# Kernel tuning notes

Hardware: AMD Instinct MI355X
Metric: run time of the kernel (lower is better)

Reference implementation:

```python
import jax, jax.numpy as jnp
import numpy as np

DIM = 512
HEADS = 16
WIN = (8, 8)
N = WIN[0] * WIN[1]  # 64 tokens per window
BW = 1024            # batch * num_windows
TABLE = (2 * WIN[0] - 1) * (2 * WIN[1] - 1)  # 225


def _relative_position_index():
    ch, cw = np.arange(WIN[0]), np.arange(WIN[1])
    coords = np.stack(np.meshgrid(ch, cw, indexing='ij'))        # [2,Wh,Ww]
    flat = coords.reshape(2, -1)                                  # [2,N]
    rel = flat[:, :, None] - flat[:, None, :]                     # [2,N,N]
    rel = rel.transpose(1, 2, 0).astype(np.int64)                 # [N,N,2]
    rel[:, :, 0] += WIN[0] - 1
    rel[:, :, 1] += WIN[1] - 1
    rel[:, :, 0] *= 2 * WIN[1] - 1
    return jnp.asarray(rel.sum(-1), dtype=jnp.int32)              # [N,N]


def setup_inputs() -> dict:
    key = jax.random.key(0)
    ks = jax.random.split(key, 8)
    s = 0.02
    return {
        'q': jax.random.normal(ks[0], (BW, N, DIM), jnp.float32),
        'wq': jax.random.normal(ks[1], (DIM, DIM), jnp.float32) * s,
        'bq': jnp.zeros((DIM,), jnp.float32),
        'wkv': jax.random.normal(ks[2], (DIM, 2 * DIM), jnp.float32) * s,
        'bkv': jnp.zeros((2 * DIM,), jnp.float32),
        'wproj': jax.random.normal(ks[3], (DIM, DIM), jnp.float32) * s,
        'bproj': jnp.zeros((DIM,), jnp.float32),
        'bias_table': jax.random.normal(ks[4], (TABLE, HEADS), jnp.float32) * s,
        'rel_pos_index': _relative_position_index(),
    }


def reference(q, wq, bq, wkv, bkv, wproj, bproj, bias_table, rel_pos_index):
    B, n, C = q.shape
    hd = C // HEADS
    scale = hd ** -0.5
    # projections (torch Linear with pre-transposed weights)
    qh = (q @ wq + bq).reshape(B, n, HEADS, hd).transpose(0, 2, 1, 3) * scale  # [B,H,N,hd]
    kv = (q @ wkv + bkv).reshape(B, n, 2, HEADS, hd)
    k = kv[:, :, 0].transpose(0, 2, 1, 3)  # [B,H,N,hd]
    v = kv[:, :, 1].transpose(0, 2, 1, 3)
    attn = jnp.einsum('bhqd,bhkd->bhqk', qh, k)                   # [B,H,N,N]
    bias = bias_table[rel_pos_index].transpose(2, 0, 1)           # [H,N,N]
    attn = jax.nn.softmax(attn + bias[None], axis=-1)
    x = jnp.einsum('bhqk,bhkd->bqhd', attn, v).reshape(B, n, C)
    x = x @ wproj + bproj
    return x, attn
```

## Files before the change

### kernel.cpp

```cpp
#include <hip/hip_runtime.h>
#include <hip/hip_bf16.h>
#include <stdint.h>

typedef __attribute__((ext_vector_type(8))) __bf16 bf16x8;
typedef __attribute__((ext_vector_type(4))) float f32x4;

#define MFMA16(a, b, c) __builtin_amdgcn_mfma_f32_16x16x32_bf16(a, b, c, 0, 0, 0)

__device__ __forceinline__ void gload16(const void* g, void* l) {
  __builtin_amdgcn_global_load_lds((const __attribute__((address_space(1))) void*)g,
                                   (__attribute__((address_space(3))) void*)l, 16, 0, 0);
}

__global__ __launch_bounds__(256) void prep_kernel(
    const float* __restrict__ wq, const float* __restrict__ bq,
    const float* __restrict__ wkv, const float* __restrict__ bkv,
    const float* __restrict__ wproj, const float* __restrict__ btab,
    const int* __restrict__ relidx,
    __bf16* __restrict__ W1t, __bf16* __restrict__ WpT,
    float* __restrict__ bias1, float* __restrict__ bias_frag) {
  const float scale = 0.17677669529663687f;
  int t = blockIdx.x * 256 + threadIdx.x;
  if (t < 786432) {
    int j = t >> 9, kk = t & 511;
    float v = (j < 512) ? wq[kk * 512 + j] * scale : wkv[kk * 1024 + (j - 512)];
    W1t[t] = (__bf16)v;
  } else if (t < 1048576) {
    int u = t - 786432;
    int j = u >> 9, kk = u & 511;
    WpT[u] = (__bf16)wproj[kk * 512 + j];
  } else if (t < 1050112) {
    int j = t - 1048576;
    bias1[j] = (j < 512) ? bq[j] * scale : bkv[j - 512];
  } else if (t < 1115648) {
    int u = t - 1050112;
    int r = u & 3, l = (u >> 2) & 63, nj = (u >> 8) & 3, mi = (u >> 10) & 3, h = u >> 12;
    int qq = mi * 16 + (l >> 4) * 4 + r;
    int nn = nj * 16 + (l & 15);
    bias_frag[u] = btab[relidx[qq * 64 + nn] * 16 + h];
  }
}

__global__ __launch_bounds__(256) void cvt_kernel(const float* __restrict__ in,
                                                  __bf16* __restrict__ out) {
  int t = blockIdx.x * 256 + threadIdx.x;
  const float4* p = (const float4*)in + (size_t)t * 2;
  float4 a = p[0], b = p[1];
  bf16x8 v = {(__bf16)a.x, (__bf16)a.y, (__bf16)a.z, (__bf16)a.w,
              (__bf16)b.x, (__bf16)b.y, (__bf16)b.z, (__bf16)b.w};
  *((bf16x8*)out + t) = v;
}

__global__ __launch_bounds__(256) void gemm1_kernel(
    const __bf16* __restrict__ A, const __bf16* __restrict__ W1t,
    const float* __restrict__ bias1,
    __bf16* __restrict__ qh, __bf16* __restrict__ kb, __bf16* __restrict__ vT) {
  __shared__ __bf16 As[128 * 32];
  __shared__ __bf16 Bs[128 * 32];
  int tid = threadIdx.x;
  int w = tid >> 6, l = tid & 63, c = l & 15, g = l >> 4;
  int wm = w >> 1, wn = w & 1;
  int bx = blockIdx.x, by = blockIdx.y;
  int r0 = by * 128, n0 = bx * 128;

  f32x4 acc[4][4] = {};
  int e0 = w * 1024 + l * 8;
  int rn0 = e0 >> 5, rk0 = e0 & 31;
  int e1 = e0 + 512;
  int rn1 = e1 >> 5, rk1 = e1 & 31;

  for (int kt = 0; kt < 16; ++kt) {
    int k0 = kt * 32;
    __syncthreads();
    gload16(A + (size_t)(r0 + rn0) * 512 + k0 + rk0, (void*)(As + w * 1024));
    gload16(A + (size_t)(r0 + rn1) * 512 + k0 + rk1, (void*)(As + w * 1024 + 512));
    gload16(W1t + (size_t)(n0 + rn0) * 512 + k0 + rk0, (void*)(Bs + w * 1024));
    gload16(W1t + (size_t)(n0 + rn1) * 512 + k0 + rk1, (void*)(Bs + w * 1024 + 512));
    __syncthreads();
    bf16x8 af[4], bfr[4];
#pragma unroll
    for (int mi = 0; mi < 4; mi++) af[mi] = *(const bf16x8*)(As + (wm * 64 + mi * 16 + c) * 32 + g * 8);
#pragma unroll
    for (int nj = 0; nj < 4; nj++) bfr[nj] = *(const bf16x8*)(Bs + (wn * 64 + nj * 16 + c) * 32 + g * 8);
#pragma unroll
    for (int mi = 0; mi < 4; mi++)
#pragma unroll
      for (int nj = 0; nj < 4; nj++)
        acc[mi][nj] = MFMA16(af[mi], bfr[nj], acc[mi][nj]);
  }

  float bia[4];
#pragma unroll
  for (int nj = 0; nj < 4; nj++) bia[nj] = bias1[n0 + wn * 64 + nj * 16 + c];
  int rowbase = r0 + wm * 64 + g * 4;
  int colbase = n0 + wn * 64 + c;
#pragma unroll
  for (int mi = 0; mi < 4; mi++) {
#pragma unroll
    for (int nj = 0; nj < 4; nj++) {
      int col = colbase + nj * 16;
      int jj = col & 511;
      int h = jj >> 5, d = jj & 31;
#pragma unroll
      for (int r = 0; r < 4; r++) {
        int row = rowbase + mi * 16 + r;
        int b = row >> 6, tok = row & 63;
        float val = acc[mi][nj][r] + bia[nj];
        size_t base = (size_t)(b * 16 + h) * 2048;
        if (bx < 4)
          qh[base + tok * 32 + d] = (__bf16)val;
        else if (bx < 8)
          kb[base + tok * 32 + d] = (__bf16)val;
        else
          vT[base + d * 64 + tok] = (__bf16)val;
      }
    }
  }
}

__global__ __launch_bounds__(64) void attn_kernel(
    const __bf16* __restrict__ qh, const __bf16* __restrict__ kb,
    const __bf16* __restrict__ vT, const float* __restrict__ bias_frag,
    float* __restrict__ attn_out, __bf16* __restrict__ xpart) {
  __shared__ __bf16 P[64 * 72];
  int bh = blockIdx.x;
  int b = bh >> 4, h = bh & 15;
  int l = threadIdx.x, c = l & 15, g = l >> 4;
  const __bf16* qp = qh + (size_t)bh * 2048;
  const __bf16* kp = kb + (size_t)bh * 2048;
  const __bf16* vp = vT + (size_t)bh * 2048;

  bf16x8 af[4], bfr[4];
#pragma unroll
  for (int mi = 0; mi < 4; mi++) af[mi] = *(const bf16x8*)(qp + (mi * 16 + c) * 32 + g * 8);
#pragma unroll
  for (int nj = 0; nj < 4; nj++) bfr[nj] = *(const bf16x8*)(kp + (nj * 16 + c) * 32 + g * 8);

  f32x4 acc[4][4];
#pragma unroll
  for (int mi = 0; mi < 4; mi++)
#pragma unroll
    for (int nj = 0; nj < 4; nj++)
      acc[mi][nj] = *(const f32x4*)(bias_frag + ((size_t)((h * 4 + mi) * 4 + nj) * 64 + l) * 4);
#pragma unroll
  for (int mi = 0; mi < 4; mi++)
#pragma unroll
    for (int nj = 0; nj < 4; nj++)
      acc[mi][nj] = MFMA16(af[mi], bfr[nj], acc[mi][nj]);

  float* ao = attn_out + (size_t)bh * 4096;
#pragma unroll
  for (int mi = 0; mi < 4; mi++) {
#pragma unroll
    for (int r = 0; r < 4; r++) {
      float m = fmaxf(fmaxf(acc[mi][0][r], acc[mi][1][r]), fmaxf(acc[mi][2][r], acc[mi][3][r]));
      m = fmaxf(m, __shfl_xor(m, 1));
      m = fmaxf(m, __shfl_xor(m, 2));
      m = fmaxf(m, __shfl_xor(m, 4));
      m = fmaxf(m, __shfl_xor(m, 8));
      float p0 = __expf(acc[mi][0][r] - m);
      float p1 = __expf(acc[mi][1][r] - m);
      float p2 = __expf(acc[mi][2][r] - m);
      float p3 = __expf(acc[mi][3][r] - m);
      float s = p0 + p1 + p2 + p3;
      s += __shfl_xor(s, 1);
      s += __shfl_xor(s, 2);
      s += __shfl_xor(s, 4);
      s += __shfl_xor(s, 8);
      float rs = 1.0f / s;
      p0 *= rs; p1 *= rs; p2 *= rs; p3 *= rs;
      int row = mi * 16 + g * 4 + r;
      ao[row * 64 + c] = p0;
      ao[row * 64 + 16 + c] = p1;
      ao[row * 64 + 32 + c] = p2;
      ao[row * 64 + 48 + c] = p3;
      P[row * 72 + c] = (__bf16)p0;
      P[row * 72 + 16 + c] = (__bf16)p1;
      P[row * 72 + 32 + c] = (__bf16)p2;
      P[row * 72 + 48 + c] = (__bf16)p3;
    }
  }
  __syncthreads();

  bf16x8 pa[4][2];
#pragma unroll
  for (int mi = 0; mi < 4; mi++)
#pragma unroll
    for (int kk = 0; kk < 2; kk++)
      pa[mi][kk] = *(const bf16x8*)(P + (mi * 16 + c) * 72 + kk * 32 + g * 8);
  bf16x8 bv[2][2];
#pragma unroll
  for (int dj = 0; dj < 2; dj++)
#pragma unroll
    for (int kk = 0; kk < 2; kk++)
      bv[dj][kk] = *(const bf16x8*)(vp + (c + 16 * dj) * 64 + kk * 32 + g * 8);
  f32x4 xacc[4][2] = {};
#pragma unroll
  for (int mi = 0; mi < 4; mi++)
#pragma unroll
    for (int dj = 0; dj < 2; dj++)
#pragma unroll
      for (int kk = 0; kk < 2; kk++)
        xacc[mi][dj] = MFMA16(pa[mi][kk], bv[dj][kk], xacc[mi][dj]);

  __bf16* xp = xpart + (size_t)b * 64 * 512 + h * 32;
#pragma unroll
  for (int mi = 0; mi < 4; mi++)
#pragma unroll
    for (int dj = 0; dj < 2; dj++)
#pragma unroll
      for (int r = 0; r < 4; r++) {
        int row = mi * 16 + g * 4 + r;
        xp[(size_t)row * 512 + dj * 16 + c] = (__bf16)xacc[mi][dj][r];
      }
}

__global__ __launch_bounds__(256) void gemm2_kernel(
    const __bf16* __restrict__ A, const __bf16* __restrict__ WpT,
    const float* __restrict__ bproj, float* __restrict__ out) {
  __shared__ __bf16 As[128 * 32];
  __shared__ __bf16 Bs[128 * 32];
  int tid = threadIdx.x;
  int w = tid >> 6, l = tid & 63, c = l & 15, g = l >> 4;
  int wm = w >> 1, wn = w & 1;
  int bx = blockIdx.x, by = blockIdx.y;
  int r0 = by * 128, n0 = bx * 128;

  f32x4 acc[4][4] = {};
  int e0 = w * 1024 + l * 8;
  int rn0 = e0 >> 5, rk0 = e0 & 31;
  int e1 = e0 + 512;
  int rn1 = e1 >> 5, rk1 = e1 & 31;

  for (int kt = 0; kt < 16; ++kt) {
    int k0 = kt * 32;
    __syncthreads();
    gload16(A + (size_t)(r0 + rn0) * 512 + k0 + rk0, (void*)(As + w * 1024));
    gload16(A + (size_t)(r0 + rn1) * 512 + k0 + rk1, (void*)(As + w * 1024 + 512));
    gload16(WpT + (size_t)(n0 + rn0) * 512 + k0 + rk0, (void*)(Bs + w * 1024));
    gload16(WpT + (size_t)(n0 + rn1) * 512 + k0 + rk1, (void*)(Bs + w * 1024 + 512));
    __syncthreads();
    bf16x8 af[4], bfr[4];
#pragma unroll
    for (int mi = 0; mi < 4; mi++) af[mi] = *(const bf16x8*)(As + (wm * 64 + mi * 16 + c) * 32 + g * 8);
#pragma unroll
    for (int nj = 0; nj < 4; nj++) bfr[nj] = *(const bf16x8*)(Bs + (wn * 64 + nj * 16 + c) * 32 + g * 8);
#pragma unroll
    for (int mi = 0; mi < 4; mi++)
#pragma unroll
      for (int nj = 0; nj < 4; nj++)
        acc[mi][nj] = MFMA16(af[mi], bfr[nj], acc[mi][nj]);
  }

  float bia[4];
#pragma unroll
  for (int nj = 0; nj < 4; nj++) bia[nj] = bproj[n0 + wn * 64 + nj * 16 + c];
  int rowbase = r0 + wm * 64 + g * 4;
  int colbase = n0 + wn * 64 + c;
#pragma unroll
  for (int mi = 0; mi < 4; mi++)
#pragma unroll
    for (int nj = 0; nj < 4; nj++)
#pragma unroll
      for (int r = 0; r < 4; r++) {
        int row = rowbase + mi * 16 + r;
        out[(size_t)row * 512 + colbase + nj * 16] = acc[mi][nj][r] + bia[nj];
      }
}

extern "C" void kernel_launch(void* const* d_in, const int* in_sizes, int n_in,
                              void* d_out, int out_size, void* d_ws, size_t ws_size,
                              hipStream_t stream) {
  const float* q = (const float*)d_in[0];
  const float* wq = (const float*)d_in[1];
  const float* bq = (const float*)d_in[2];
  const float* wkv = (const float*)d_in[3];
  const float* bkv = (const float*)d_in[4];
  const float* wproj = (const float*)d_in[5];
  const float* bproj = (const float*)d_in[6];
  const float* btab = (const float*)d_in[7];
  const int* relidx = (const int*)d_in[8];

  float* x_out = (float*)d_out;
  float* attn_out = x_out + 33554432;
  __bf16* qbf = (__bf16*)attn_out;

  char* ws = (char*)d_ws;
  __bf16* qh = (__bf16*)(ws);
  __bf16* kb = (__bf16*)(ws + 67108864);
  __bf16* vT = (__bf16*)(ws + 134217728);
  __bf16* xpart = (__bf16*)(ws + 201326592);
  __bf16* W1t = (__bf16*)(ws + 268435456);
  __bf16* WpT = (__bf16*)(ws + 270008320);
  float* bias1 = (float*)(ws + 270532608);
  float* bfrag = (float*)(ws + 270538752);

  hipLaunchKernelGGL(prep_kernel, dim3(4358), dim3(256), 0, stream,
                     wq, bq, wkv, bkv, wproj, btab, relidx, W1t, WpT, bias1, bfrag);
  hipLaunchKernelGGL(cvt_kernel, dim3(16384), dim3(256), 0, stream, q, qbf);
  hipLaunchKernelGGL(gemm1_kernel, dim3(12, 512), dim3(256), 0, stream,
                     qbf, W1t, bias1, qh, kb, vT);
  hipLaunchKernelGGL(attn_kernel, dim3(16384), dim3(64), 0, stream,
                     qh, kb, vT, bfrag, attn_out, xpart);
  hipLaunchKernelGGL(gemm2_kernel, dim3(4, 512), dim3(256), 0, stream,
                     xpart, WpT, bproj, x_out);
}
```

Measured before the change: 848.5 us.

## Store V untransposed, transpose via LDS in attention, remap GEMM blocks per XCD

The QKV GEMM now writes V in the same token-major layout as Q and K, which removes the strided transposed scatter stores in its epilogue. The attention kernel loads V with coalesced 16-byte reads and stages it in a padded LDS tile, then gathers the transposed MFMA operand element by element. Both GEMMs also swap the 2D grid for a 1D grid whose block index is remapped so consecutive tiles land on the same XCD, aiming for better L2 reuse. The cost is extra LDS traffic and scalar LDS reads in the attention kernel.

Measured after the change: 801.5 us. 1.06x faster.

```diff
diff --git a/kernel.cpp b/kernel.cpp
--- a/kernel.cpp
+++ b/kernel.cpp
@@ -54,13 +54,14 @@
 __global__ __launch_bounds__(256) void gemm1_kernel(
     const __bf16* __restrict__ A, const __bf16* __restrict__ W1t,
     const float* __restrict__ bias1,
-    __bf16* __restrict__ qh, __bf16* __restrict__ kb, __bf16* __restrict__ vT) {
+    __bf16* __restrict__ qh, __bf16* __restrict__ kb, __bf16* __restrict__ vv) {
   __shared__ __bf16 As[128 * 32];
   __shared__ __bf16 Bs[128 * 32];
   int tid = threadIdx.x;
   int w = tid >> 6, l = tid & 63, c = l & 15, g = l >> 4;
   int wm = w >> 1, wn = w & 1;
-  int bx = blockIdx.x, by = blockIdx.y;
+  int bflat = (blockIdx.x & 7) * 768 + (blockIdx.x >> 3);
+  int bx = bflat % 12, by = bflat / 12;
   int r0 = by * 128, n0 = bx * 128;
 
   f32x4 acc[4][4] = {};
@@ -89,6 +90,8 @@
         acc[mi][nj] = MFMA16(af[mi], bfr[nj], acc[mi][nj]);
   }
 
+  __bf16* dst = (bx < 4) ? qh : (bx < 8) ? kb : vv;
+
   float bia[4];
 #pragma unroll
   for (int nj = 0; nj < 4; nj++) bia[nj] = bias1[n0 + wn * 64 + nj * 16 + c];
@@ -106,13 +109,7 @@
         int row = rowbase + mi * 16 + r;
         int b = row >> 6, tok = row & 63;
         float val = acc[mi][nj][r] + bia[nj];
-        size_t base = (size_t)(b * 16 + h) * 2048;
-        if (bx < 4)
-          qh[base + tok * 32 + d] = (__bf16)val;
-        else if (bx < 8)
-          kb[base + tok * 32 + d] = (__bf16)val;
-        else
-          vT[base + d * 64 + tok] = (__bf16)val;
+        dst[(size_t)(b * 16 + h) * 2048 + tok * 32 + d] = (__bf16)val;
       }
     }
   }
@@ -120,15 +117,21 @@
 
 __global__ __launch_bounds__(64) void attn_kernel(
     const __bf16* __restrict__ qh, const __bf16* __restrict__ kb,
-    const __bf16* __restrict__ vT, const float* __restrict__ bias_frag,
+    const __bf16* __restrict__ vv, const float* __restrict__ bias_frag,
     float* __restrict__ attn_out, __bf16* __restrict__ xpart) {
   __shared__ __bf16 P[64 * 72];
+  __shared__ __bf16 Vlds[64 * 34];
   int bh = blockIdx.x;
   int b = bh >> 4, h = bh & 15;
   int l = threadIdx.x, c = l & 15, g = l >> 4;
   const __bf16* qp = qh + (size_t)bh * 2048;
   const __bf16* kp = kb + (size_t)bh * 2048;
-  const __bf16* vp = vT + (size_t)bh * 2048;
+  const __bf16* vp = vv + (size_t)bh * 2048;
+
+  uint4 vst[4];
+  const uint4* vg = (const uint4*)vp;
+#pragma unroll
+  for (int i = 0; i < 4; i++) vst[i] = vg[l + 64 * i];
 
   bf16x8 af[4], bfr[4];
 #pragma unroll
@@ -142,6 +145,15 @@
 #pragma unroll
     for (int nj = 0; nj < 4; nj++)
       acc[mi][nj] = *(const f32x4*)(bias_frag + ((size_t)((h * 4 + mi) * 4 + nj) * 64 + l) * 4);
+
+#pragma unroll
+  for (int i = 0; i < 4; i++) {
+    int ch = l + 64 * i;
+    int row = ch >> 2, pos = ch & 3;
+    uint32_t* pw = (uint32_t*)&Vlds[row * 34 + pos * 8];
+    pw[0] = vst[i].x; pw[1] = vst[i].y; pw[2] = vst[i].z; pw[3] = vst[i].w;
+  }
+
 #pragma unroll
   for (int mi = 0; mi < 4; mi++)
 #pragma unroll
@@ -188,12 +200,16 @@
 #pragma unroll
     for (int kk = 0; kk < 2; kk++)
       pa[mi][kk] = *(const bf16x8*)(P + (mi * 16 + c) * 72 + kk * 32 + g * 8);
+
   bf16x8 bv[2][2];
 #pragma unroll
   for (int dj = 0; dj < 2; dj++)
 #pragma unroll
     for (int kk = 0; kk < 2; kk++)
-      bv[dj][kk] = *(const bf16x8*)(vp + (c + 16 * dj) * 64 + kk * 32 + g * 8);
+#pragma unroll
+      for (int e = 0; e < 8; e++)
+        bv[dj][kk][e] = Vlds[(32 * kk + 8 * g + e) * 34 + 16 * dj + c];
+
   f32x4 xacc[4][2] = {};
 #pragma unroll
   for (int mi = 0; mi < 4; mi++)
@@ -223,7 +239,8 @@
   int tid = threadIdx.x;
   int w = tid >> 6, l = tid & 63, c = l & 15, g = l >> 4;
   int wm = w >> 1, wn = w & 1;
-  int bx = blockIdx.x, by = blockIdx.y;
+  int bflat = (blockIdx.x & 7) * 256 + (blockIdx.x >> 3);
+  int bx = bflat & 3, by = bflat >> 2;
   int r0 = by * 128, n0 = bx * 128;
 
   f32x4 acc[4][4] = {};
@@ -288,7 +305,7 @@
   char* ws = (char*)d_ws;
   __bf16* qh = (__bf16*)(ws);
   __bf16* kb = (__bf16*)(ws + 67108864);
-  __bf16* vT = (__bf16*)(ws + 134217728);
+  __bf16* vv = (__bf16*)(ws + 134217728);
   __bf16* xpart = (__bf16*)(ws + 201326592);
   __bf16* W1t = (__bf16*)(ws + 268435456);
   __bf16* WpT = (__bf16*)(ws + 270008320);
@@ -298,10 +315,10 @@
   hipLaunchKernelGGL(prep_kernel, dim3(4358), dim3(256), 0, stream,
                      wq, bq, wkv, bkv, wproj, btab, relidx, W1t, WpT, bias1, bfrag);
   hipLaunchKernelGGL(cvt_kernel, dim3(16384), dim3(256), 0, stream, q, qbf);
-  hipLaunchKernelGGL(gemm1_kernel, dim3(12, 512), dim3(256), 0, stream,
-                     qbf, W1t, bias1, qh, kb, vT);
+  hipLaunchKernelGGL(gemm1_kernel, dim3(6144), dim3(256), 0, stream,
+                     qbf, W1t, bias1, qh, kb, vv);
   hipLaunchKernelGGL(attn_kernel, dim3(16384), dim3(64), 0, stream,
-                     qh, kb, vT, bfrag, attn_out, xpart);
-  hipLaunchKernelGGL(gemm2_kernel, dim3(4, 512), dim3(256), 0, stream,
+                     qh, kb, vv, bfrag, attn_out, xpart);
+  hipLaunchKernelGGL(gemm2_kernel, dim3(2048), dim3(256), 0, stream,
                      xpart, WpT, bproj, x_out);
 }
```
